# Performance work log

Hardware: AMD Instinct MI355X
Metric: run time of the kernel (lower is better)

The kernel has to match this reference:

```python
import jax, jax.numpy as jnp
import numpy as np

BATCH, SEQ, INPUT, HIDDEN = 256, 512, 128, 256

def setup_inputs() -> dict:
    key = jax.random.key(0)
    ks = jax.random.split(key, 7)
    s = 1.0 / np.sqrt(INPUT + HIDDEN)
    return {
        "X": jax.random.normal(ks[0], (BATCH, SEQ, INPUT), dtype=jnp.float32),
        "W_z": jax.random.normal(ks[1], (HIDDEN, INPUT + HIDDEN), dtype=jnp.float32) * s,
        "b_z": jax.random.normal(ks[2], (HIDDEN,), dtype=jnp.float32) * s,
        "W_r": jax.random.normal(ks[3], (HIDDEN, INPUT + HIDDEN), dtype=jnp.float32) * s,
        "b_r": jax.random.normal(ks[4], (HIDDEN,), dtype=jnp.float32) * s,
        "W_c": jax.random.normal(ks[5], (HIDDEN, INPUT + HIDDEN), dtype=jnp.float32) * s,
        "b_c": jax.random.normal(ks[6], (HIDDEN,), dtype=jnp.float32) * s,
    }

def reference(X, W_z, b_z, W_r, b_r, W_c, b_c):
    # X: [batch, seq, input] -> scan over time (seq, batch, input)
    Xt = jnp.transpose(X, (1, 0, 2))
    h0 = jnp.zeros((X.shape[0], HIDDEN), dtype=X.dtype)

    def step(h, x):
        hx = jnp.concatenate([h, x], axis=1)          # [B, H+I] (cat order: h then x)
        z = jax.nn.sigmoid(hx @ W_z.T + b_z)          # update gate
        r = jax.nn.sigmoid(hx @ W_r.T + b_r)          # reset gate
        rhx = jnp.concatenate([r * h, x], axis=1)
        cand = jnp.tanh(rhx @ W_c.T + b_c)            # candidate state
        h_new = (1.0 - z) * h + z * cand
        return h_new, h_new

    _, h_history = jax.lax.scan(step, h0, Xt)
    return h_history  # [seq, batch, hidden]
```

## Files before the change

### kernel.cpp

```cpp
#include <hip/hip_runtime.h>
#include <hip/hip_bf16.h>


typedef float f32x4 __attribute__((ext_vector_type(4)));
typedef short s16x8 __attribute__((ext_vector_type(8)));

#define SEQ 512
#define NB  256
#define NI  128
#define NH  256
#define WROW 384
#define GX_BYTES ((size_t)201326592)
#define WTAB_BYTES ((size_t)196608)

static __device__ inline float bf2f(unsigned short s) {
    unsigned u = ((unsigned)s) << 16;
    return __builtin_bit_cast(float, u);
}
static __device__ inline unsigned pkbf(float a, float b) {
    __hip_bfloat162 h = __float22bfloat162_rn(make_float2(a, b));
    unsigned r;
    __builtin_memcpy(&r, &h, 4);
    return r;
}
static __device__ inline s16x8 pk8(f32x4 f0, f32x4 f1) {
    uint4 u;
    u.x = pkbf(f0[0], f0[1]);
    u.y = pkbf(f0[2], f0[3]);
    u.z = pkbf(f1[0], f1[1]);
    u.w = pkbf(f1[2], f1[3]);
    return __builtin_bit_cast(s16x8, u);
}
static __device__ inline float fexp2(float x) {
#if __has_builtin(__builtin_amdgcn_exp2f)
    return __builtin_amdgcn_exp2f(x);
#else
    return exp2f(x);
#endif
}
static __device__ inline float frcp(float x) {
#if __has_builtin(__builtin_amdgcn_rcpf)
    return __builtin_amdgcn_rcpf(x);
#else
    return 1.0f / x;
#endif
}
static __device__ inline float sigm(float x)  { return frcp(1.0f + fexp2(-1.44269504f * x)); }
static __device__ inline float tanh_(float x) { return 1.0f - 2.0f * frcp(1.0f + fexp2(2.88539008f * x)); }

static __device__ inline void lds_barrier() {
    asm volatile("s_waitcnt lgkmcnt(0)\n\ts_barrier" ::: "memory");
}

static __device__ inline int prow(int m) {
    return 2 * (m >> 2) + (m & 1) + 8 * ((m >> 1) & 1);
}

__global__ __launch_bounds__(256, 1) void gru_wprep(
    const float* __restrict__ Wz, const float* __restrict__ Wr, const float* __restrict__ Wc,
    unsigned short* __restrict__ wtab)
{
    int task = blockIdx.x * 256 + threadIdx.x;
    int l  = task & 63;
    int fr = task >> 6;
    int v  = fr / 48;
    int f  = fr - v * 48;
    int g  = f >> 4, tt = (f >> 2) & 3, kt = f & 3;
    const float* Wp = (g == 0) ? Wz : (g == 1) ? Wr : Wc;
    int j = v * 64 + tt * 16 + (l & 15);
    const float* src = Wp + (size_t)j * WROW + 256 + kt * 32 + (l >> 4) * 8;
    f32x4 f0 = *(const f32x4*)src;
    f32x4 f1 = *(const f32x4*)(src + 4);
    *(s16x8*)(wtab + (size_t)task * 8) = pk8(f0, f1);
}

__global__ __launch_bounds__(256, 1) void gru_xpre(
    const float* __restrict__ X,
    const float* __restrict__ bz, const float* __restrict__ br, const float* __restrict__ bc,
    const unsigned short* __restrict__ wtab,
    unsigned short* __restrict__ Gx)
{
    __shared__ unsigned short x_lds[32768];
    const int tid  = threadIdx.x;
    const int t    = blockIdx.x;
    const int l    = tid & 63;
    const int v    = tid >> 6;
    const int quad = l >> 4;
    const int n    = l & 15;

    for (int i = tid; i < 4096; i += 256) {
        int row = i >> 4, c = i & 15;
        const float* src = X + (size_t)(row * SEQ + t) * NI + c * 8;
        f32x4 f0 = *(const f32x4*)(src);
        f32x4 f1 = *(const f32x4*)(src + 4);
        *(s16x8*)(&x_lds[row * 128 + ((c ^ (row & 15)) << 3)]) = pk8(f0, f1);
    }

    s16x8 Bf[3][4][4];
    float bias[3][4];
    {
        const unsigned short* wt = wtab + ((size_t)v * 48 * 64 + l) * 8;
#pragma unroll
        for (int g = 0; g < 3; ++g)
#pragma unroll
            for (int tt = 0; tt < 4; ++tt)
#pragma unroll
                for (int kt = 0; kt < 4; ++kt)
                    Bf[g][tt][kt] = *(const s16x8*)(wt + (size_t)(g * 16 + tt * 4 + kt) * 64 * 8);
        const float* bp[3] = {bz, br, bc};
#pragma unroll
        for (int g = 0; g < 3; ++g)
#pragma unroll
            for (int tt = 0; tt < 4; ++tt)
                bias[g][tt] = bp[g][v * 64 + tt * 16 + n];
    }
    __syncthreads();

    const int rowA = l & 15;
#pragma unroll 1
    for (int mt = 0; mt < 16; ++mt) {
        f32x4 acc[3][4];
        f32x4 z4 = {0.f, 0.f, 0.f, 0.f};
#pragma unroll
        for (int g = 0; g < 3; ++g)
#pragma unroll
            for (int tt = 0; tt < 4; ++tt) acc[g][tt] = z4;

#pragma unroll
        for (int kt = 0; kt < 4; ++kt) {
            int row = mt * 16 + rowA;
            s16x8 a = *(const s16x8*)(&x_lds[row * 128 + (((kt * 4 + quad) ^ rowA) << 3)]);
#pragma unroll
            for (int g = 0; g < 3; ++g)
#pragma unroll
                for (int tt = 0; tt < 4; ++tt)
                    acc[g][tt] = __builtin_amdgcn_mfma_f32_16x16x32_bf16(a, Bf[g][tt][kt], acc[g][tt], 0, 0, 0);
        }

#pragma unroll
        for (int g = 0; g < 3; ++g)
#pragma unroll
            for (int tt = 0; tt < 4; ++tt) {
                float b = bias[g][tt];
                uint2 d;
                d.x = pkbf(acc[g][tt][0] + b, acc[g][tt][1] + b);
                d.y = pkbf(acc[g][tt][2] + b, acc[g][tt][3] + b);
                int chunk = (((t * 16 + mt) * 4 + v) * 3 + g) * 4 + tt;
                *(uint2*)((char*)Gx + (size_t)chunk * 512 + l * 8) = d;
            }
    }
}

__global__ __launch_bounds__(256, 1) void gru_xpre_gather(
    const float* __restrict__ X,
    const float* __restrict__ Wz, const float* __restrict__ bz,
    const float* __restrict__ Wr, const float* __restrict__ br,
    const float* __restrict__ Wc, const float* __restrict__ bc,
    unsigned short* __restrict__ Gx)
{
    __shared__ unsigned short x_lds[32768];
    const int tid  = threadIdx.x;
    const int t    = blockIdx.x;
    const int l    = tid & 63;
    const int v    = tid >> 6;
    const int quad = l >> 4;
    const int n    = l & 15;

    for (int i = tid; i < 4096; i += 256) {
        int row = i >> 4, c = i & 15;
        const float* src = X + (size_t)(row * SEQ + t) * NI + c * 8;
        f32x4 f0 = *(const f32x4*)(src);
        f32x4 f1 = *(const f32x4*)(src + 4);
        *(s16x8*)(&x_lds[row * 128 + ((c ^ (row & 15)) << 3)]) = pk8(f0, f1);
    }

    const float* Wp[3] = {Wz, Wr, Wc};
    const float* bp[3] = {bz, br, bc};
    s16x8 Bf[3][4][4];
    float bias[3][4];
#pragma unroll
    for (int g = 0; g < 3; ++g) {
#pragma unroll
        for (int tt = 0; tt < 4; ++tt) {
            int j = v * 64 + tt * 16 + n;
            bias[g][tt] = bp[g][j];
#pragma unroll
            for (int kt = 0; kt < 4; ++kt) {
                const float* src = Wp[g] + j * WROW + 256 + kt * 32 + quad * 8;
                f32x4 f0 = *(const f32x4*)(src);
                f32x4 f1 = *(const f32x4*)(src + 4);
                Bf[g][tt][kt] = pk8(f0, f1);
            }
        }
    }
    __syncthreads();

    const int rowA = l & 15;
#pragma unroll 1
    for (int mt = 0; mt < 16; ++mt) {
        f32x4 acc[3][4];
        f32x4 z4 = {0.f, 0.f, 0.f, 0.f};
#pragma unroll
        for (int g = 0; g < 3; ++g)
#pragma unroll
            for (int tt = 0; tt < 4; ++tt) acc[g][tt] = z4;

#pragma unroll
        for (int kt = 0; kt < 4; ++kt) {
            int row = mt * 16 + rowA;
            s16x8 a = *(const s16x8*)(&x_lds[row * 128 + (((kt * 4 + quad) ^ rowA) << 3)]);
#pragma unroll
            for (int g = 0; g < 3; ++g)
#pragma unroll
                for (int tt = 0; tt < 4; ++tt)
                    acc[g][tt] = __builtin_amdgcn_mfma_f32_16x16x32_bf16(a, Bf[g][tt][kt], acc[g][tt], 0, 0, 0);
        }

#pragma unroll
        for (int g = 0; g < 3; ++g)
#pragma unroll
            for (int tt = 0; tt < 4; ++tt) {
                float b = bias[g][tt];
                uint2 d;
                d.x = pkbf(acc[g][tt][0] + b, acc[g][tt][1] + b);
                d.y = pkbf(acc[g][tt][2] + b, acc[g][tt][3] + b);
                int chunk = (((t * 16 + mt) * 4 + v) * 3 + g) * 4 + tt;
                *(uint2*)((char*)Gx + (size_t)chunk * 512 + l * 8) = d;
            }
    }
}

__global__ __launch_bounds__(512, 2) void gru_seq(
    const float* __restrict__ Wz, const float* __restrict__ Wr, const float* __restrict__ Wc,
    const unsigned short* __restrict__ Gx,
    float* __restrict__ out)
{
    __shared__ unsigned short wc_lds[32768];
    __shared__ unsigned short h_lds[16][264];
    __shared__ unsigned short rh_lds[16][264];

    const int tid  = threadIdx.x;
    const int wg   = blockIdx.x;
    const int l    = tid & 63;
    const int w    = tid >> 6;
    const int quad = l >> 4;
    const int n    = l & 15;
    const int rowR = prow(n);

    const float* Wp2[2] = {Wz, Wr};
    s16x8 Wf[2][2][8];
#pragma unroll
    for (int g = 0; g < 2; ++g)
#pragma unroll
        for (int tt = 0; tt < 2; ++tt)
#pragma unroll
            for (int kt = 0; kt < 8; ++kt) {
                int j = w * 32 + tt * 16 + n;
                const float* src = Wp2[g] + j * WROW + kt * 32 + quad * 8;
                f32x4 f0 = *(const f32x4*)(src);
                f32x4 f1 = *(const f32x4*)(src + 4);
                Wf[g][tt][kt] = pk8(f0, f1);
            }

    s16x8 Wcr[2][4];
#pragma unroll
    for (int tt = 0; tt < 2; ++tt)
#pragma unroll
        for (int kt = 0; kt < 4; ++kt) {
            int j = w * 32 + tt * 16 + n;
            const float* src = Wc + j * WROW + kt * 32 + quad * 8;
            f32x4 f0 = *(const f32x4*)(src);
            f32x4 f1 = *(const f32x4*)(src + 4);
            Wcr[tt][kt] = pk8(f0, f1);
        }

    for (int idx = tid; idx < 4096; idx += 512) {
        int fr = idx >> 6, ln = idx & 63;
        int jb = fr >> 2, ktm = fr & 3;
        int j = jb * 16 + (ln & 15);
        int k = (ktm + 4) * 32 + (ln >> 4) * 8;
        const float* src = Wc + j * WROW + k;
        f32x4 f0 = *(const f32x4*)(src);
        f32x4 f1 = *(const f32x4*)(src + 4);
        *(s16x8*)(&wc_lds[idx * 8]) = pk8(f0, f1);
    }

    {
        unsigned short* hz = &h_lds[0][0];
        for (int i = tid; i < 16 * 264; i += 512) hz[i] = 0;
    }
    float hreg[2][4];
#pragma unroll
    for (int tt = 0; tt < 2; ++tt)
#pragma unroll
        for (int r = 0; r < 4; ++r) hreg[tt][r] = 0.0f;
    __syncthreads();

    const char* gxbase = (const char*)Gx
        + (size_t)(((wg * 4 + (w >> 1)) * 12 + (w & 1) * 2) * 512) + l * 8;
    float* outp = out + (size_t)(wg * 16 + quad * 4) * 256 + w * 32 + n;
    const f32x4 z4 = {0.f, 0.f, 0.f, 0.f};

    int wr0 = prow(quad * 4 + 0), wr1 = prow(quad * 4 + 1);
    int wr2 = prow(quad * 4 + 2), wr3 = prow(quad * 4 + 3);

    uint2 ga[6];
#pragma unroll
    for (int i = 0; i < 6; ++i)
        ga[i] = *(const uint2*)(gxbase + (i >> 1) * 2048 + (i & 1) * 512);

#pragma unroll 1
    for (int t = 0; t < SEQ; ++t) {
        const char* gbn = gxbase + (size_t)(t + 1 < SEQ ? t + 1 : t) * 393216;

        f32x4 accZ[2], accR[2];
#pragma unroll
        for (int tt = 0; tt < 2; ++tt) { accZ[tt] = z4; accR[tt] = z4; }
        __builtin_amdgcn_s_setprio(1);
#pragma unroll
        for (int kt = 0; kt < 8; ++kt) {
            s16x8 a = *(const s16x8*)(&h_lds[rowR][kt * 32 + quad * 8]);
#pragma unroll
            for (int tt = 0; tt < 2; ++tt) {
                accZ[tt] = __builtin_amdgcn_mfma_f32_16x16x32_bf16(a, Wf[0][tt][kt], accZ[tt], 0, 0, 0);
                accR[tt] = __builtin_amdgcn_mfma_f32_16x16x32_bf16(a, Wf[1][tt][kt], accR[tt], 0, 0, 0);
            }
        }
        __builtin_amdgcn_s_setprio(0);

        float zs[2][4];
        {
            float gzf[2][4], grf[2][4];
#pragma unroll
            for (int tt = 0; tt < 2; ++tt) {
                uint2 gz = ga[tt], gr = ga[2 + tt];
                gzf[tt][0] = bf2f((unsigned short)(gz.x & 0xffffu));
                gzf[tt][1] = bf2f((unsigned short)(gz.x >> 16));
                gzf[tt][2] = bf2f((unsigned short)(gz.y & 0xffffu));
                gzf[tt][3] = bf2f((unsigned short)(gz.y >> 16));
                grf[tt][0] = bf2f((unsigned short)(gr.x & 0xffffu));
                grf[tt][1] = bf2f((unsigned short)(gr.x >> 16));
                grf[tt][2] = bf2f((unsigned short)(gr.y & 0xffffu));
                grf[tt][3] = bf2f((unsigned short)(gr.y >> 16));
            }
#pragma unroll
            for (int i = 0; i < 4; ++i)
                ga[i] = *(const uint2*)(gbn + (i >> 1) * 2048 + (i & 1) * 512);
#pragma unroll
            for (int tt = 0; tt < 2; ++tt) {
                float rh[4];
#pragma unroll
                for (int r = 0; r < 4; ++r) {
                    float zv = sigm(accZ[tt][r] + gzf[tt][r]);
                    float rv = sigm(accR[tt][r] + grf[tt][r]);
                    zs[tt][r] = zv;
                    rh[r] = rv * hreg[tt][r];
                }
                unsigned pa = pkbf(rh[0], rh[1]);
                unsigned pb = pkbf(rh[2], rh[3]);
                const int col = w * 32 + tt * 16 + n;
                rh_lds[wr0][col] = (unsigned short)pa;
                rh_lds[wr1][col] = (unsigned short)(pa >> 16);
                rh_lds[wr2][col] = (unsigned short)pb;
                rh_lds[wr3][col] = (unsigned short)(pb >> 16);
            }
        }
        lds_barrier();

        f32x4 accC[2];
#pragma unroll
        for (int tt = 0; tt < 2; ++tt) accC[tt] = z4;
        __builtin_amdgcn_s_setprio(1);
#pragma unroll
        for (int kt = 0; kt < 8; ++kt) {
            s16x8 a = *(const s16x8*)(&rh_lds[rowR][kt * 32 + quad * 8]);
#pragma unroll
            for (int tt = 0; tt < 2; ++tt) {
                s16x8 b = (kt < 4)
                    ? Wcr[tt][kt]
                    : *(const s16x8*)(&wc_lds[(((w * 2 + tt) * 4 + (kt - 4)) * 64 + l) * 8]);
                accC[tt] = __builtin_amdgcn_mfma_f32_16x16x32_bf16(a, b, accC[tt], 0, 0, 0);
            }
        }
        __builtin_amdgcn_s_setprio(0);

        {
            float gcf[2][4];
#pragma unroll
            for (int tt = 0; tt < 2; ++tt) {
                uint2 gc = ga[4 + tt];
                gcf[tt][0] = bf2f((unsigned short)(gc.x & 0xffffu));
                gcf[tt][1] = bf2f((unsigned short)(gc.x >> 16));
                gcf[tt][2] = bf2f((unsigned short)(gc.y & 0xffffu));
                gcf[tt][3] = bf2f((unsigned short)(gc.y >> 16));
            }
#pragma unroll
            for (int i = 4; i < 6; ++i)
                ga[i] = *(const uint2*)(gbn + 4096 + (i & 1) * 512);
            float* op = outp + (size_t)t * 65536;
#pragma unroll
            for (int tt = 0; tt < 2; ++tt) {
                float hn4[4];
#pragma unroll
                for (int r = 0; r < 4; ++r) {
                    float cv = tanh_(accC[tt][r] + gcf[tt][r]);
                    float h  = hreg[tt][r];
                    float hn = fmaf(zs[tt][r], cv - h, h);
                    hreg[tt][r] = hn;
                    hn4[r] = hn;
                    op[r * 256 + tt * 16] = hn;
                }
                unsigned pa = pkbf(hn4[0], hn4[1]);
                unsigned pb = pkbf(hn4[2], hn4[3]);
                const int col = w * 32 + tt * 16 + n;
                h_lds[wr0][col] = (unsigned short)pa;
                h_lds[wr1][col] = (unsigned short)(pa >> 16);
                h_lds[wr2][col] = (unsigned short)pb;
                h_lds[wr3][col] = (unsigned short)(pb >> 16);
            }
        }
        lds_barrier();
    }
}

__global__ __launch_bounds__(1024, 1) void gru_fallback(
    const float* __restrict__ X,
    const float* __restrict__ Wz, const float* __restrict__ bz,
    const float* __restrict__ Wr, const float* __restrict__ br,
    const float* __restrict__ Wc, const float* __restrict__ bc,
    float* __restrict__ out)
{
    __shared__ float h_s[16][257];
    __shared__ float rh_s[16][257];
    __shared__ float x_s[16][128];
    const int tid = threadIdx.x;
    const int wg = blockIdx.x, b0 = wg * 16;
    const int m = tid >> 6, jq = tid & 63;
    for (int i = tid; i < 16 * 257; i += 1024) (&h_s[0][0])[i] = 0.0f;
    __syncthreads();
    for (int t = 0; t < SEQ; ++t) {
        for (int i = tid; i < 2048; i += 1024) {
            int row = i >> 7, k = i & 127;
            x_s[row][k] = X[(size_t)((b0 + row) * SEQ + t) * NI + k];
        }
        __syncthreads();
        float zv[4];
        for (int jj = 0; jj < 4; ++jj) {
            int j = jj * 64 + jq;
            float az = bz[j], ar = br[j];
            for (int k = 0; k < 256; ++k) { float h = h_s[m][k]; az += h * Wz[j * WROW + k]; ar += h * Wr[j * WROW + k]; }
            for (int k = 0; k < 128; ++k) { float x = x_s[m][k]; az += x * Wz[j * WROW + 256 + k]; ar += x * Wr[j * WROW + 256 + k]; }
            float z = sigm(az), r = sigm(ar);
            zv[jj] = z;
            rh_s[m][j] = r * h_s[m][j];
        }
        __syncthreads();
        float hn[4];
        for (int jj = 0; jj < 4; ++jj) {
            int j = jj * 64 + jq;
            float ac = bc[j];
            for (int k = 0; k < 256; ++k) ac += rh_s[m][k] * Wc[j * WROW + k];
            for (int k = 0; k < 128; ++k) ac += x_s[m][k] * Wc[j * WROW + 256 + k];
            float c = tanh_(ac);
            float h = h_s[m][j];
            hn[jj] = fmaf(zv[jj], c - h, h);
        }
        __syncthreads();
        for (int jj = 0; jj < 4; ++jj) {
            int j = jj * 64 + jq;
            h_s[m][j] = hn[jj];
            out[(size_t)(t * 256 + b0 + m) * 256 + j] = hn[jj];
        }
        __syncthreads();
    }
}

extern "C" void kernel_launch(void* const* d_in, const int* in_sizes, int n_in,
                              void* d_out, int out_size, void* d_ws, size_t ws_size,
                              hipStream_t stream) {
    const float* X  = (const float*)d_in[0];
    const float* Wz = (const float*)d_in[1];
    const float* bz = (const float*)d_in[2];
    const float* Wr = (const float*)d_in[3];
    const float* br = (const float*)d_in[4];
    const float* Wc = (const float*)d_in[5];
    const float* bc = (const float*)d_in[6];
    float* out = (float*)d_out;

    if (ws_size >= GX_BYTES + WTAB_BYTES) {
        unsigned short* Gx   = (unsigned short*)d_ws;
        unsigned short* wtab = (unsigned short*)((char*)d_ws + GX_BYTES);
        gru_wprep<<<48, 256, 0, stream>>>(Wz, Wr, Wc, wtab);
        gru_xpre<<<512, 256, 0, stream>>>(X, bz, br, bc, wtab, Gx);
        gru_seq<<<16, 512, 0, stream>>>(Wz, Wr, Wc, Gx, out);
    } else if (ws_size >= GX_BYTES) {
        unsigned short* Gx = (unsigned short*)d_ws;
        gru_xpre_gather<<<512, 256, 0, stream>>>(X, Wz, bz, Wr, br, Wc, bc, Gx);
        gru_seq<<<16, 512, 0, stream>>>(Wz, Wr, Wc, Gx, out);
    } else {
        gru_fallback<<<16, 1024, 0, stream>>>(X, Wz, bz, Wr, br, Wc, bc, out);
    }
}
```

Measured before the change: 1.196 ms.

## Split x-projection across more blocks and pack h stores via DPP swaps

The input-projection kernel now splits each timestep's batch into four quarters, giving four times as many blocks. It uses a quarter of the LDS, loops over gates with a smaller register footprint, and allows two blocks per CU to improve occupancy. In the sequential kernel the permuted row mapping is replaced by DPP lane swaps, so each lane writes packed 32-bit pairs to LDS instead of four 16-bit scalar stores. The s_setprio hints around the MFMA loops are also removed. The added DPP and select work sits on the per-step critical path, and the gate weights are reloaded per gate in the projection kernel.

```diff
diff --git a/kernel.cpp b/kernel.cpp
--- a/kernel.cpp
+++ b/kernel.cpp
@@ -31,6 +31,11 @@
     u.w = pkbf(f1[2], f1[3]);
     return __builtin_bit_cast(s16x8, u);
 }
+static __device__ inline float dpp_xor1(float x) {
+    int i = __builtin_bit_cast(int, x);
+    int p = __builtin_amdgcn_mov_dpp(i, 0xB1, 0xF, 0xF, true);
+    return __builtin_bit_cast(float, p);
+}
 static __device__ inline float fexp2(float x) {
 #if __has_builtin(__builtin_amdgcn_exp2f)
     return __builtin_amdgcn_exp2f(x);
@@ -50,10 +55,6 @@
 
 static __device__ inline void lds_barrier() {
     asm volatile("s_waitcnt lgkmcnt(0)\n\ts_barrier" ::: "memory");
-}
-
-static __device__ inline int prow(int m) {
-    return 2 * (m >> 2) + (m & 1) + 8 * ((m >> 1) & 1);
 }
 
 __global__ __launch_bounds__(256, 1) void gru_wprep(
@@ -74,13 +75,83 @@
     *(s16x8*)(wtab + (size_t)task * 8) = pk8(f0, f1);
 }
 
-__global__ __launch_bounds__(256, 1) void gru_xpre(
+__global__ __launch_bounds__(256, 2) void gru_xpre(
     const float* __restrict__ X,
     const float* __restrict__ bz, const float* __restrict__ br, const float* __restrict__ bc,
     const unsigned short* __restrict__ wtab,
     unsigned short* __restrict__ Gx)
 {
-    __shared__ unsigned short x_lds[32768];
+    __shared__ __align__(16) unsigned short x_lds[8192];
+    const int tid  = threadIdx.x;
+    const int t    = blockIdx.x >> 2;
+    const int mq   = blockIdx.x & 3;
+    const int l    = tid & 63;
+    const int v    = tid >> 6;
+    const int quad = l >> 4;
+    const int n    = l & 15;
+
+    for (int i = tid; i < 1024; i += 256) {
+        int lr = i >> 4, c = i & 15;
+        const float* src = X + (size_t)((mq * 64 + lr) * SEQ + t) * NI + c * 8;
+        f32x4 f0 = *(const f32x4*)(src);
+        f32x4 f1 = *(const f32x4*)(src + 4);
+        *(s16x8*)(&x_lds[lr * 128 + ((c ^ (lr & 15)) << 3)]) = pk8(f0, f1);
+    }
+    __syncthreads();
+
+    const float* bp[3] = {bz, br, bc};
+    const int rowA = n;
+#pragma unroll 1
+    for (int g = 0; g < 3; ++g) {
+        s16x8 Bf[4][4];
+        float bias[4];
+#pragma unroll
+        for (int tt = 0; tt < 4; ++tt) {
+            bias[tt] = bp[g][v * 64 + tt * 16 + n];
+#pragma unroll
+            for (int kt = 0; kt < 4; ++kt)
+                Bf[tt][kt] = *(const s16x8*)(wtab
+                    + ((size_t)(v * 48 + g * 16 + tt * 4 + kt) * 64 + l) * 8);
+        }
+
+#pragma unroll 1
+        for (int mtl = 0; mtl < 4; ++mtl) {
+            const int mt = mq * 4 + mtl;
+            f32x4 acc[4];
+            const f32x4 z4 = {0.f, 0.f, 0.f, 0.f};
+#pragma unroll
+            for (int tt = 0; tt < 4; ++tt) acc[tt] = z4;
+
+#pragma unroll
+            for (int kt = 0; kt < 4; ++kt) {
+                s16x8 a = *(const s16x8*)(&x_lds[(mtl * 16 + rowA) * 128
+                                                 + (((kt * 4 + quad) ^ rowA) << 3)]);
+#pragma unroll
+                for (int tt = 0; tt < 4; ++tt)
+                    acc[tt] = __builtin_amdgcn_mfma_f32_16x16x32_bf16(a, Bf[tt][kt], acc[tt], 0, 0, 0);
+            }
+
+#pragma unroll
+            for (int tt = 0; tt < 4; ++tt) {
+                float b = bias[tt];
+                uint2 d;
+                d.x = pkbf(acc[tt][0] + b, acc[tt][1] + b);
+                d.y = pkbf(acc[tt][2] + b, acc[tt][3] + b);
+                int chunk = (((t * 16 + mt) * 4 + v) * 3 + g) * 4 + tt;
+                *(uint2*)((char*)Gx + (size_t)chunk * 512 + l * 8) = d;
+            }
+        }
+    }
+}
+
+__global__ __launch_bounds__(256, 1) void gru_xpre_gather(
+    const float* __restrict__ X,
+    const float* __restrict__ Wz, const float* __restrict__ bz,
+    const float* __restrict__ Wr, const float* __restrict__ br,
+    const float* __restrict__ Wc, const float* __restrict__ bc,
+    unsigned short* __restrict__ Gx)
+{
+    __shared__ __align__(16) unsigned short x_lds[32768];
     const int tid  = threadIdx.x;
     const int t    = blockIdx.x;
     const int l    = tid & 63;
@@ -96,23 +167,24 @@
         *(s16x8*)(&x_lds[row * 128 + ((c ^ (row & 15)) << 3)]) = pk8(f0, f1);
     }
 
+    const float* Wp[3] = {Wz, Wr, Wc};
+    const float* bp[3] = {bz, br, bc};
     s16x8 Bf[3][4][4];
     float bias[3][4];
-    {
-        const unsigned short* wt = wtab + ((size_t)v * 48 * 64 + l) * 8;
-#pragma unroll
-        for (int g = 0; g < 3; ++g)
-#pragma unroll
-            for (int tt = 0; tt < 4; ++tt)
-#pragma unroll
-                for (int kt = 0; kt < 4; ++kt)
-                    Bf[g][tt][kt] = *(const s16x8*)(wt + (size_t)(g * 16 + tt * 4 + kt) * 64 * 8);
-        const float* bp[3] = {bz, br, bc};
-#pragma unroll
-        for (int g = 0; g < 3; ++g)
-#pragma unroll
-            for (int tt = 0; tt < 4; ++tt)
-                bias[g][tt] = bp[g][v * 64 + tt * 16 + n];
+#pragma unroll
+    for (int g = 0; g < 3; ++g) {
+#pragma unroll
+        for (int tt = 0; tt < 4; ++tt) {
+            int j = v * 64 + tt * 16 + n;
+            bias[g][tt] = bp[g][j];
+#pragma unroll
+            for (int kt = 0; kt < 4; ++kt) {
+                const float* src = Wp[g] + j * WROW + 256 + kt * 32 + quad * 8;
+                f32x4 f0 = *(const f32x4*)(src);
+                f32x4 f1 = *(const f32x4*)(src + 4);
+                Bf[g][tt][kt] = pk8(f0, f1);
+            }
+        }
     }
     __syncthreads();
 
@@ -151,93 +223,14 @@
     }
 }
 
-__global__ __launch_bounds__(256, 1) void gru_xpre_gather(
-    const float* __restrict__ X,
-    const float* __restrict__ Wz, const float* __restrict__ bz,
-    const float* __restrict__ Wr, const float* __restrict__ br,
-    const float* __restrict__ Wc, const float* __restrict__ bc,
-    unsigned short* __restrict__ Gx)
-{
-    __shared__ unsigned short x_lds[32768];
-    const int tid  = threadIdx.x;
-    const int t    = blockIdx.x;
-    const int l    = tid & 63;
-    const int v    = tid >> 6;
-    const int quad = l >> 4;
-    const int n    = l & 15;
-
-    for (int i = tid; i < 4096; i += 256) {
-        int row = i >> 4, c = i & 15;
-        const float* src = X + (size_t)(row * SEQ + t) * NI + c * 8;
-        f32x4 f0 = *(const f32x4*)(src);
-        f32x4 f1 = *(const f32x4*)(src + 4);
-        *(s16x8*)(&x_lds[row * 128 + ((c ^ (row & 15)) << 3)]) = pk8(f0, f1);
-    }
-
-    const float* Wp[3] = {Wz, Wr, Wc};
-    const float* bp[3] = {bz, br, bc};
-    s16x8 Bf[3][4][4];
-    float bias[3][4];
-#pragma unroll
-    for (int g = 0; g < 3; ++g) {
-#pragma unroll
-        for (int tt = 0; tt < 4; ++tt) {
-            int j = v * 64 + tt * 16 + n;
-            bias[g][tt] = bp[g][j];
-#pragma unroll
-            for (int kt = 0; kt < 4; ++kt) {
-                const float* src = Wp[g] + j * WROW + 256 + kt * 32 + quad * 8;
-                f32x4 f0 = *(const f32x4*)(src);
-                f32x4 f1 = *(const f32x4*)(src + 4);
-                Bf[g][tt][kt] = pk8(f0, f1);
-            }
-        }
-    }
-    __syncthreads();
-
-    const int rowA = l & 15;
-#pragma unroll 1
-    for (int mt = 0; mt < 16; ++mt) {
-        f32x4 acc[3][4];
-        f32x4 z4 = {0.f, 0.f, 0.f, 0.f};
-#pragma unroll
-        for (int g = 0; g < 3; ++g)
-#pragma unroll
-            for (int tt = 0; tt < 4; ++tt) acc[g][tt] = z4;
-
-#pragma unroll
-        for (int kt = 0; kt < 4; ++kt) {
-            int row = mt * 16 + rowA;
-            s16x8 a = *(const s16x8*)(&x_lds[row * 128 + (((kt * 4 + quad) ^ rowA) << 3)]);
-#pragma unroll
-            for (int g = 0; g < 3; ++g)
-#pragma unroll
-                for (int tt = 0; tt < 4; ++tt)
-                    acc[g][tt] = __builtin_amdgcn_mfma_f32_16x16x32_bf16(a, Bf[g][tt][kt], acc[g][tt], 0, 0, 0);
-        }
-
-#pragma unroll
-        for (int g = 0; g < 3; ++g)
-#pragma unroll
-            for (int tt = 0; tt < 4; ++tt) {
-                float b = bias[g][tt];
-                uint2 d;
-                d.x = pkbf(acc[g][tt][0] + b, acc[g][tt][1] + b);
-                d.y = pkbf(acc[g][tt][2] + b, acc[g][tt][3] + b);
-                int chunk = (((t * 16 + mt) * 4 + v) * 3 + g) * 4 + tt;
-                *(uint2*)((char*)Gx + (size_t)chunk * 512 + l * 8) = d;
-            }
-    }
-}
-
 __global__ __launch_bounds__(512, 2) void gru_seq(
     const float* __restrict__ Wz, const float* __restrict__ Wr, const float* __restrict__ Wc,
     const unsigned short* __restrict__ Gx,
     float* __restrict__ out)
 {
-    __shared__ unsigned short wc_lds[32768];
-    __shared__ unsigned short h_lds[16][264];
-    __shared__ unsigned short rh_lds[16][264];
+    __shared__ __align__(16) unsigned short wc_lds[32768];
+    __shared__ __align__(16) unsigned short h_lds[16][264];
+    __shared__ __align__(16) unsigned short rh_lds[16][264];
 
     const int tid  = threadIdx.x;
     const int wg   = blockIdx.x;
@@ -245,7 +238,7 @@
     const int w    = tid >> 6;
     const int quad = l >> 4;
     const int n    = l & 15;
-    const int rowR = prow(n);
+    const int rowA = n;
 
     const float* Wp2[2] = {Wz, Wr};
     s16x8 Wf[2][2][8];
@@ -301,8 +294,11 @@
     float* outp = out + (size_t)(wg * 16 + quad * 4) * 256 + w * 32 + n;
     const f32x4 z4 = {0.f, 0.f, 0.f, 0.f};
 
-    int wr0 = prow(quad * 4 + 0), wr1 = prow(quad * 4 + 1);
-    int wr2 = prow(quad * 4 + 2), wr3 = prow(quad * 4 + 3);
+    const int odd   = n & 1;
+    const int dcol0 = w * 16 + (n >> 1);
+    const int wrow  = quad * 4 + (odd ? 2 : 0);
+    unsigned* h32  = (unsigned*)&h_lds[0][0];
+    unsigned* rh32 = (unsigned*)&rh_lds[0][0];
 
     uint2 ga[6];
 #pragma unroll
@@ -316,17 +312,15 @@
         f32x4 accZ[2], accR[2];
 #pragma unroll
         for (int tt = 0; tt < 2; ++tt) { accZ[tt] = z4; accR[tt] = z4; }
-        __builtin_amdgcn_s_setprio(1);
 #pragma unroll
         for (int kt = 0; kt < 8; ++kt) {
-            s16x8 a = *(const s16x8*)(&h_lds[rowR][kt * 32 + quad * 8]);
+            s16x8 a = *(const s16x8*)(&h_lds[rowA][kt * 32 + quad * 8]);
 #pragma unroll
             for (int tt = 0; tt < 2; ++tt) {
                 accZ[tt] = __builtin_amdgcn_mfma_f32_16x16x32_bf16(a, Wf[0][tt][kt], accZ[tt], 0, 0, 0);
                 accR[tt] = __builtin_amdgcn_mfma_f32_16x16x32_bf16(a, Wf[1][tt][kt], accR[tt], 0, 0, 0);
             }
         }
-        __builtin_amdgcn_s_setprio(0);
 
         float zs[2][4];
         {
@@ -356,13 +350,13 @@
                     zs[tt][r] = zv;
                     rh[r] = rv * hreg[tt][r];
                 }
-                unsigned pa = pkbf(rh[0], rh[1]);
-                unsigned pb = pkbf(rh[2], rh[3]);
-                const int col = w * 32 + tt * 16 + n;
-                rh_lds[wr0][col] = (unsigned short)pa;
-                rh_lds[wr1][col] = (unsigned short)(pa >> 16);
-                rh_lds[wr2][col] = (unsigned short)pb;
-                rh_lds[wr3][col] = (unsigned short)(pb >> 16);
+                float p0 = dpp_xor1(rh[0]), p1 = dpp_xor1(rh[1]);
+                float p2 = dpp_xor1(rh[2]), p3 = dpp_xor1(rh[3]);
+                unsigned val0 = pkbf(odd ? p2 : rh[0], odd ? rh[2] : p0);
+                unsigned val1 = pkbf(odd ? p3 : rh[1], odd ? rh[3] : p1);
+                int base = wrow * 132 + dcol0 + tt * 8;
+                rh32[base]       = val0;
+                rh32[base + 132] = val1;
             }
         }
         lds_barrier();
@@ -370,10 +364,9 @@
         f32x4 accC[2];
 #pragma unroll
         for (int tt = 0; tt < 2; ++tt) accC[tt] = z4;
-        __builtin_amdgcn_s_setprio(1);
 #pragma unroll
         for (int kt = 0; kt < 8; ++kt) {
-            s16x8 a = *(const s16x8*)(&rh_lds[rowR][kt * 32 + quad * 8]);
+            s16x8 a = *(const s16x8*)(&rh_lds[rowA][kt * 32 + quad * 8]);
 #pragma unroll
             for (int tt = 0; tt < 2; ++tt) {
                 s16x8 b = (kt < 4)
@@ -382,7 +375,6 @@
                 accC[tt] = __builtin_amdgcn_mfma_f32_16x16x32_bf16(a, b, accC[tt], 0, 0, 0);
             }
         }
-        __builtin_amdgcn_s_setprio(0);
 
         {
             float gcf[2][4];
@@ -410,13 +402,13 @@
                     hn4[r] = hn;
                     op[r * 256 + tt * 16] = hn;
                 }
-                unsigned pa = pkbf(hn4[0], hn4[1]);
-                unsigned pb = pkbf(hn4[2], hn4[3]);
-                const int col = w * 32 + tt * 16 + n;
-                h_lds[wr0][col] = (unsigned short)pa;
-                h_lds[wr1][col] = (unsigned short)(pa >> 16);
-                h_lds[wr2][col] = (unsigned short)pb;
-                h_lds[wr3][col] = (unsigned short)(pb >> 16);
+                float p0 = dpp_xor1(hn4[0]), p1 = dpp_xor1(hn4[1]);
+                float p2 = dpp_xor1(hn4[2]), p3 = dpp_xor1(hn4[3]);
+                unsigned val0 = pkbf(odd ? p2 : hn4[0], odd ? hn4[2] : p0);
+                unsigned val1 = pkbf(odd ? p3 : hn4[1], odd ? hn4[3] : p1);
+                int base = wrow * 132 + dcol0 + tt * 8;
+                h32[base]       = val0;
+                h32[base + 132] = val1;
             }
         }
         lds_barrier();
@@ -491,7 +483,7 @@
         unsigned short* Gx   = (unsigned short*)d_ws;
         unsigned short* wtab = (unsigned short*)((char*)d_ws + GX_BYTES);
         gru_wprep<<<48, 256, 0, stream>>>(Wz, Wr, Wc, wtab);
-        gru_xpre<<<512, 256, 0, stream>>>(X, bz, br, bc, wtab, Gx);
+        gru_xpre<<<2048, 256, 0, stream>>>(X, bz, br, bc, wtab, Gx);
         gru_seq<<<16, 512, 0, stream>>>(Wz, Wr, Wc, Gx, out);
     } else if (ws_size >= GX_BYTES) {
         unsigned short* Gx = (unsigned short*)d_ws;
```

Result: faster. 1.162 ms (-2.8%).
